# Kernel tuning notes

Measured on AMD Instinct MI355X. Metric: run time of the kernel, lower is better.

## Reference

```python
import jax, jax.numpy as jnp
import numpy as np
from jax import lax

CONV3_NUM = 5
CONV1_NUM = 1
NEG_SLOPE = 0.2


def _leaky(x):
    return jnp.where(x >= 0, x, NEG_SLOPE * x)


def _per_sample_conv(x, k, b, pad):
    # x: [B,3,H,W], k: [B,3,3,kh,kw] (OIHW per sample), b: [B,3]
    def one(xi, ki, bi):
        y = lax.conv_general_dilated(
            xi[None], ki, (1, 1), ((pad, pad), (pad, pad)),
            dimension_numbers=("NCHW", "OIHW", "NCHW"))[0]
        return y + bi[:, None, None]
    return jax.vmap(one)(x, k, b)


def _conv3x3_block(x, feat):
    B = x.shape[0]
    k = feat[:, :81].reshape(B, 3, 3, 3, 3)
    b = feat[:, 81:84]
    return _leaky(x + _per_sample_conv(x, k, b, 1))


def _conv1x1_block(x, feat):
    B = x.shape[0]
    k = feat[:, :9].reshape(B, 3, 3, 1, 1)
    b = feat[:, 9:12]
    return _leaky(x + _per_sample_conv(x, k, b, 0))


def _att_map(f, h, w, xi):
    # f: [B,20]; h,w: [1,1,H,W]; xi: [B,1,H,W]  -> cubic trivariate polynomial
    c = lambda i: f[:, i][:, None, None, None]
    h2 = h * h; h3 = h2 * h
    w2 = w * w; w3 = w2 * w
    x2 = xi * xi; x3 = x2 * xi
    return (c(0) * h3 + c(1) * h2 * w + c(2) * h2 * xi + c(3) * h2
            + c(4) * h * w2 + c(5) * h * w * xi + c(6) * h * w
            + c(7) * h * x2 + c(8) * h * xi + c(9) * h
            + c(10) * w3 + c(11) * w2 * xi + c(12) * w2
            + c(13) * w * x2 + c(14) * w * xi + c(15) * w
            + c(16) * x3 + c(17) * x2 + c(18) * xi + c(19))


def setup_inputs() -> dict:
    key = jax.random.key(0)
    k1, k2, k3 = jax.random.split(key, 3)
    x = jax.random.normal(k1, (8, 3, 1024, 1024), dtype=jnp.float32)
    thumb_x = jax.random.normal(k2, (8, 3, 256, 256), dtype=jnp.float32)
    # meta() is an external CNN predicting per-sample params; we materialize its
    # output directly (scaled small for numerical stability of the conv stack).
    feature = jax.random.normal(k3, (8, 492), dtype=jnp.float32) * 0.05
    return {"x": x, "thumb_x": thumb_x, "feature": feature}


def reference(x, thumb_x, feature):
    B, _, H, W = x.shape
    residual = x
    for i in range(CONV3_NUM):
        x = _conv3x3_block(x, feature[:, i * 84:(i + 1) * 84])
    off = CONV3_NUM * 84
    for i in range(CONV1_NUM):
        x = _conv1x1_block(x, feature[:, off + i * 12:off + (i + 1) * 12])
    off = off + CONV1_NUM * 12
    x = residual + x
    dt = x.dtype
    h_mat = jnp.broadcast_to((jnp.arange(H, dtype=dt) / H)[None, None, :, None], (1, 1, H, W))
    w_mat = jnp.broadcast_to((jnp.arange(W, dtype=dt) / W)[None, None, None, :], (1, 1, H, W))
    atts = [_att_map(feature[:, off + 20 * c:off + 20 * (c + 1)], h_mat, w_mat, x[:, c:c + 1])
            for c in range(3)]
    att = jnp.concatenate(atts, axis=1)
    x = x * (1 + att)
    # location is None => thumbnail branch is skipped, thumb_x returned as-is
    return (x, thumb_x)
```

## Files before the change

### kernel.cpp

```cpp
#include <hip/hip_runtime.h>
#include <hip/hip_fp16.h>

typedef unsigned int uint;
typedef _Float16 h2 __attribute__((ext_vector_type(2)));


#define ROWS   42
#define W_U    23
#define CHP_U  (ROWS*W_U)
#define BUF_U  (3*CHP_U)

__device__ __forceinline__ h2   U2H(uint u) { return __builtin_bit_cast(h2, u); }
__device__ __forceinline__ uint H2U(h2 h)   { return __builtin_bit_cast(uint, h); }

__global__ void prep_weights(const float* __restrict__ feat, uint* __restrict__ wtab)
{
    const int b = blockIdx.x;
    const int t = threadIdx.x;
    float w = 0.f;
    bool valid = false;
    if (t < 405) {
        int l = t / 81, r = t % 81;
        int ic = r / 27; r %= 27;
        int ky = r / 9;  r %= 9;
        int oc = r / 3;
        int kx = r % 3;
        w = feat[b * 492 + l * 84 + ((oc * 3 + ic) * 3 + ky) * 3 + kx];
        valid = true;
    } else if (t < 420) {
        int i = t - 405;
        w = feat[b * 492 + (i / 3) * 84 + 81 + (i % 3)];
        valid = true;
    }
    if (valid) {
        _Float16 h = (_Float16)w;
        h2 hh = { h, h };
        wtab[b * 448 + t] = H2U(hh);
    }
}

__global__ __launch_bounds__(512, 8) void fused_net(
    const float* __restrict__ xin,
    const float* __restrict__ thumb,
    const float* __restrict__ feat,
    const uint*  __restrict__ wtab,
    float* __restrict__ out)
{
    const int tid = threadIdx.x;

    if (blockIdx.x == 32) {
        const int part = blockIdx.y + 32 * blockIdx.z;
        const float4* s4 = (const float4*)thumb;
        float4* d4 = (float4*)(out + 25165824ull);
        const int n4 = 1572864 / 4;
        for (int i = part * 512 + tid; i < n4; i += 256 * 512)
            d4[i] = s4[i];
        return;
    }

    const int gx0 = blockIdx.x * 32;
    const int gy0 = blockIdx.y * 32;
    const int b   = blockIdx.z;
    const float* wf = feat + b * 492;
    const uint*  wt = wtab + b * 448;

    __shared__ uint lds[2 * BUF_U + 8];
    uint* b0 = lds;
    uint* b1 = lds + BUF_U + 4;

    const float* xb = xin + ((size_t)(b * 3) << 20);
    for (int idx = tid; idx < BUF_U; idx += 512) {
        int ch  = idx / CHP_U;
        int rem = idx - ch * CHP_U;
        int row = rem / W_U;
        int u   = rem - row * W_U;
        int gy = gy0 - 5 + row;
        int gx = gx0 - 6 + 2 * u;
        float f0 = 0.f, f1 = 0.f;
        if ((unsigned)gy < 1024u) {
            const float* rp = xb + (ch << 20) + (gy << 10);
            if ((unsigned)gx < 1024u)       f0 = rp[gx];
            if ((unsigned)(gx + 1) < 1024u) f1 = rp[gx + 1];
        }
        b0[idx] = __builtin_bit_cast(uint, __builtin_amdgcn_cvt_pkrtz(f0, f1));
    }
    __syncthreads();

    const int erow = tid >> 4;
    const int col2 = (tid & 15) << 1;
    const int ub   = (5 + erow) * W_U + 3 + (col2 >> 1);
    uint resu[3];
    #pragma unroll
    for (int ch = 0; ch < 3; ++ch) resu[ch] = b0[ch * CHP_U + ub];

    const h2 c02 = { (_Float16)0.2f, (_Float16)0.2f };
    const h2 z2  = { (_Float16)0.f,  (_Float16)0.f  };

    #pragma unroll
    for (int l = 0; l < 5; ++l) {
        uint* sb = (l & 1) ? b1 : b0;
        uint* db = (l & 1) ? b0 : b1;
        const int S   = 40 - 2 * l;
        const int xs  = (S + 3) >> 2;
        const int nst = S * xs;
        const int oy  = l + 1;
        const int EX  = (l + 2) & ~1;
        if (tid < nst) {
            const int r  = tid / xs;
            const int c  = tid - r * xs;
            const int y  = oy + r;
            const int x0 = EX + 4 * c;
            const int bu = (x0 >> 1) - 1;
            const int gy  = gy0 - 5 + y;
            const int gxA = gx0 - 6 + x0;
            const uint mrow = ((unsigned)gy < 1024u) ? 0xffffffffu : 0u;
            const uint mA = mrow & ((((unsigned)gxA       < 1024u) ? 0x0000ffffu : 0u) |
                                    (((unsigned)(gxA + 1) < 1024u) ? 0xffff0000u : 0u));
            const uint mB = mrow & ((((unsigned)(gxA + 2) < 1024u) ? 0x0000ffffu : 0u) |
                                    (((unsigned)(gxA + 3) < 1024u) ? 0xffff0000u : 0u));

            h2 accA[3], accB[3];
            #pragma unroll
            for (int oc = 0; oc < 3; ++oc) {
                h2 bi = U2H(wt[405 + l * 3 + oc]);
                accA[oc] = bi; accB[oc] = bi;
            }
            uint cA[3], cB[3];
            #pragma unroll
            for (int ic = 0; ic < 3; ++ic) {
                const int ai = ic * CHP_U + (y - 1) * W_U + bu;
                #pragma unroll
                for (int ky = 0; ky < 3; ++ky) {
                    const int a = ai + ky * W_U;
                    uint u0 = sb[a], u1 = sb[a + 1], u2 = sb[a + 2], u3 = sb[a + 3];
                    uint X01 = (u0 >> 16) | (u1 << 16);
                    uint X12 = (u1 >> 16) | (u2 << 16);
                    uint X23 = (u2 >> 16) | (u3 << 16);
                    if (ky == 1) { cA[ic] = u1; cB[ic] = u2; }
                    const int wb = l * 81 + (ic * 3 + ky) * 9;
                    #pragma unroll
                    for (int oc = 0; oc < 3; ++oc) {
                        h2 w0 = U2H(wt[wb + oc * 3 + 0]);
                        h2 w1 = U2H(wt[wb + oc * 3 + 1]);
                        h2 w2 = U2H(wt[wb + oc * 3 + 2]);
                        accA[oc] = __builtin_elementwise_fma(w0, U2H(X01), accA[oc]);
                        accA[oc] = __builtin_elementwise_fma(w1, U2H(u1),  accA[oc]);
                        accA[oc] = __builtin_elementwise_fma(w2, U2H(X12), accA[oc]);
                        accB[oc] = __builtin_elementwise_fma(w0, U2H(X12), accB[oc]);
                        accB[oc] = __builtin_elementwise_fma(w1, U2H(u2),  accB[oc]);
                        accB[oc] = __builtin_elementwise_fma(w2, U2H(X23), accB[oc]);
                    }
                }
            }
            const int ob = y * W_U + (x0 >> 1);
            #pragma unroll
            for (int oc = 0; oc < 3; ++oc) {
                h2 vA = accA[oc] + U2H(cA[oc]);
                h2 vB = accB[oc] + U2H(cB[oc]);
                vA = __builtin_elementwise_fma(c02, __builtin_elementwise_min(vA, z2),
                                               __builtin_elementwise_max(vA, z2));
                vB = __builtin_elementwise_fma(c02, __builtin_elementwise_min(vB, z2),
                                               __builtin_elementwise_max(vB, z2));
                db[oc * CHP_U + ob]     = H2U(vA) & mA;
                db[oc * CHP_U + ob + 1] = H2U(vB) & mB;
            }
        }
        __syncthreads();
    }

    float x5f[3][2], resf[3][2];
    #pragma unroll
    for (int ch = 0; ch < 3; ++ch) {
        h2 hr = U2H(resu[ch]);
        resf[ch][0] = (float)hr.x; resf[ch][1] = (float)hr.y;
        h2 hx = U2H(b1[ch * CHP_U + ub]);
        x5f[ch][0] = (float)hx.x; x5f[ch][1] = (float)hx.y;
    }
    const int gy = gy0 + erow;
    const float h1 = (float)gy * (1.0f / 1024.0f);
    const float h2v = h1 * h1, h3 = h2v * h1;
    float* outb = out + ((size_t)(b * 3) << 20);
    float tmp[3][2];
    #pragma unroll
    for (int j = 0; j < 2; ++j) {
        const float wc = (float)(gx0 + col2 + j) * (1.0f / 1024.0f);
        const float w2 = wc * wc, w3 = w2 * wc;
        const float hw = h1 * wc, h2w = h2v * wc, hw2 = h1 * w2;
        #pragma unroll
        for (int oc = 0; oc < 3; ++oc) {
            float s = x5f[oc][j] + wf[429 + oc]
                    + wf[420 + oc * 3 + 0] * x5f[0][j]
                    + wf[420 + oc * 3 + 1] * x5f[1][j]
                    + wf[420 + oc * 3 + 2] * x5f[2][j];
            s = s >= 0.f ? s : 0.2f * s;
            const float xf = resf[oc][j] + s;
            const float x1 = xf, x2 = x1 * x1, x3 = x2 * x1;
            const float* cf = wf + 432 + oc * 20;
            float att =
                cf[0] * h3 + cf[1] * h2w + cf[2] * h2v * x1 + cf[3] * h2v +
                cf[4] * hw2 + cf[5] * hw * x1 + cf[6] * hw + cf[7] * h1 * x2 +
                cf[8] * h1 * x1 + cf[9] * h1 + cf[10] * w3 + cf[11] * w2 * x1 +
                cf[12] * w2 + cf[13] * wc * x2 + cf[14] * wc * x1 + cf[15] * wc +
                cf[16] * x3 + cf[17] * x2 + cf[18] * x1 + cf[19];
            tmp[oc][j] = xf * (1.f + att);
        }
    }
    #pragma unroll
    for (int oc = 0; oc < 3; ++oc) {
        float2 v = {tmp[oc][0], tmp[oc][1]};
        *(float2*)&outb[((size_t)oc << 20) + ((size_t)gy << 10) + (gx0 + col2)] = v;
    }
}

extern "C" void kernel_launch(void* const* d_in, const int* in_sizes, int n_in,
                              void* d_out, int out_size, void* d_ws, size_t ws_size,
                              hipStream_t stream) {
    const float* x     = (const float*)d_in[0];
    const float* thumb = (const float*)d_in[1];
    const float* feat  = (const float*)d_in[2];
    float* out = (float*)d_out;
    uint* wtab = (uint*)d_ws;

    prep_weights<<<dim3(8), 448, 0, stream>>>(feat, wtab);
    dim3 grid(33, 32, 8);
    fused_net<<<grid, 512, 0, stream>>>(x, thumb, feat, wtab, out);
}
```

Baseline: 299.2 us.

## Compute two output rows per thread in conv layers, vectorize loads, specialize edge tiles

Each thread now computes a 2-row by 4-column patch. It reads 4 input rows per channel instead of 6, which cuts LDS loads and shift ops for the overlapping vertical window. The tile load uses float2 global reads, with a fast path for interior tiles that skips bounds checks. Masking is applied only on edge tiles, and the row stride is padded from 23 to 26 to change LDS bank mapping. LeakyReLU becomes max(v, 0.2v) and the residual add is folded into the accumulators. Fewer threads are active per layer and register pressure per thread goes up.

```diff
diff --git a/kernel.cpp b/kernel.cpp
--- a/kernel.cpp
+++ b/kernel.cpp
@@ -6,7 +6,8 @@
 
 
 #define ROWS   42
-#define W_U    23
+#define W_U    26
+#define W_REAL 23
 #define CHP_U  (ROWS*W_U)
 #define BUF_U  (3*CHP_U)
 
@@ -61,6 +62,7 @@
     const int gx0 = blockIdx.x * 32;
     const int gy0 = blockIdx.y * 32;
     const int b   = blockIdx.z;
+    const bool edge = (gx0 == 0) | (gx0 == 992) | (gy0 == 0) | (gy0 == 992);
     const float* wf = feat + b * 492;
     const uint*  wt = wtab + b * 448;
 
@@ -69,20 +71,32 @@
     uint* b1 = lds + BUF_U + 4;
 
     const float* xb = xin + ((size_t)(b * 3) << 20);
-    for (int idx = tid; idx < BUF_U; idx += 512) {
-        int ch  = idx / CHP_U;
-        int rem = idx - ch * CHP_U;
-        int row = rem / W_U;
-        int u   = rem - row * W_U;
-        int gy = gy0 - 5 + row;
-        int gx = gx0 - 6 + 2 * u;
-        float f0 = 0.f, f1 = 0.f;
-        if ((unsigned)gy < 1024u) {
-            const float* rp = xb + (ch << 20) + (gy << 10);
-            if ((unsigned)gx < 1024u)       f0 = rp[gx];
-            if ((unsigned)(gx + 1) < 1024u) f1 = rp[gx + 1];
-        }
-        b0[idx] = __builtin_bit_cast(uint, __builtin_amdgcn_cvt_pkrtz(f0, f1));
+    if (!edge) {
+        for (int idx = tid; idx < 3 * ROWS * W_REAL; idx += 512) {
+            int ch  = idx / (ROWS * W_REAL);
+            int rem = idx - ch * (ROWS * W_REAL);
+            int row = rem / W_REAL;
+            int u   = rem - row * W_REAL;
+            const float2 f = *(const float2*)(xb + ((size_t)ch << 20) +
+                                              ((size_t)(gy0 - 5 + row) << 10) +
+                                              (gx0 - 6 + 2 * u));
+            b0[ch * CHP_U + row * W_U + u] =
+                __builtin_bit_cast(uint, __builtin_amdgcn_cvt_pkrtz(f.x, f.y));
+        }
+    } else {
+        for (int idx = tid; idx < 3 * ROWS * W_REAL; idx += 512) {
+            int ch  = idx / (ROWS * W_REAL);
+            int rem = idx - ch * (ROWS * W_REAL);
+            int row = rem / W_REAL;
+            int u   = rem - row * W_REAL;
+            const int gy = gy0 - 5 + row;
+            const int gx = gx0 - 6 + 2 * u;
+            float2 f = {0.f, 0.f};
+            if ((unsigned)gy < 1024u && (unsigned)gx < 1024u)
+                f = *(const float2*)(xb + ((size_t)ch << 20) + ((size_t)gy << 10) + gx);
+            b0[ch * CHP_U + row * W_U + u] =
+                __builtin_bit_cast(uint, __builtin_amdgcn_cvt_pkrtz(f.x, f.y));
+        }
     }
     __syncthreads();
 
@@ -94,75 +108,97 @@
     for (int ch = 0; ch < 3; ++ch) resu[ch] = b0[ch * CHP_U + ub];
 
     const h2 c02 = { (_Float16)0.2f, (_Float16)0.2f };
-    const h2 z2  = { (_Float16)0.f,  (_Float16)0.f  };
 
     #pragma unroll
     for (int l = 0; l < 5; ++l) {
         uint* sb = (l & 1) ? b1 : b0;
         uint* db = (l & 1) ? b0 : b1;
         const int S   = 40 - 2 * l;
+        const int R   = S >> 1;
         const int xs  = (S + 3) >> 2;
-        const int nst = S * xs;
+        const int nst = R * xs;
         const int oy  = l + 1;
         const int EX  = (l + 2) & ~1;
         if (tid < nst) {
             const int r  = tid / xs;
             const int c  = tid - r * xs;
-            const int y  = oy + r;
+            const int y0 = oy + 2 * r;
             const int x0 = EX + 4 * c;
             const int bu = (x0 >> 1) - 1;
-            const int gy  = gy0 - 5 + y;
-            const int gxA = gx0 - 6 + x0;
-            const uint mrow = ((unsigned)gy < 1024u) ? 0xffffffffu : 0u;
-            const uint mA = mrow & ((((unsigned)gxA       < 1024u) ? 0x0000ffffu : 0u) |
-                                    (((unsigned)(gxA + 1) < 1024u) ? 0xffff0000u : 0u));
-            const uint mB = mrow & ((((unsigned)(gxA + 2) < 1024u) ? 0x0000ffffu : 0u) |
-                                    (((unsigned)(gxA + 3) < 1024u) ? 0xffff0000u : 0u));
-
-            h2 accA[3], accB[3];
+
+            h2 accA[2][3], accB[2][3];
             #pragma unroll
             for (int oc = 0; oc < 3; ++oc) {
-                h2 bi = U2H(wt[405 + l * 3 + oc]);
-                accA[oc] = bi; accB[oc] = bi;
+                const h2 bi = U2H(wt[405 + l * 3 + oc]);
+                accA[0][oc] = bi; accA[1][oc] = bi;
+                accB[0][oc] = bi; accB[1][oc] = bi;
             }
-            uint cA[3], cB[3];
             #pragma unroll
             for (int ic = 0; ic < 3; ++ic) {
-                const int ai = ic * CHP_U + (y - 1) * W_U + bu;
+                const int ai = ic * CHP_U + (y0 - 1) * W_U + bu;
                 #pragma unroll
-                for (int ky = 0; ky < 3; ++ky) {
-                    const int a = ai + ky * W_U;
-                    uint u0 = sb[a], u1 = sb[a + 1], u2 = sb[a + 2], u3 = sb[a + 3];
-                    uint X01 = (u0 >> 16) | (u1 << 16);
-                    uint X12 = (u1 >> 16) | (u2 << 16);
-                    uint X23 = (u2 >> 16) | (u3 << 16);
-                    if (ky == 1) { cA[ic] = u1; cB[ic] = u2; }
-                    const int wb = l * 81 + (ic * 3 + ky) * 9;
+                for (int t = 0; t < 4; ++t) {
+                    const int a = ai + t * W_U;
+                    const uint u0 = sb[a], u1 = sb[a + 1], u2 = sb[a + 2], u3 = sb[a + 3];
+                    const h2 X01 = U2H((u0 >> 16) | (u1 << 16));
+                    const h2 C1  = U2H(u1);
+                    const h2 X12 = U2H((u1 >> 16) | (u2 << 16));
+                    const h2 C2  = U2H(u2);
+                    const h2 X23 = U2H((u2 >> 16) | (u3 << 16));
+                    #pragma unroll
+                    for (int j = 0; j < 2; ++j) {
+                        const int ky = t - j;
+                        if (0 <= ky && ky <= 2) {
+                            const int wb = l * 81 + (ic * 3 + ky) * 9;
+                            #pragma unroll
+                            for (int oc = 0; oc < 3; ++oc) {
+                                const h2 w0 = U2H(wt[wb + oc * 3 + 0]);
+                                const h2 w1 = U2H(wt[wb + oc * 3 + 1]);
+                                const h2 w2 = U2H(wt[wb + oc * 3 + 2]);
+                                accA[j][oc] = __builtin_elementwise_fma(w0, X01, accA[j][oc]);
+                                accA[j][oc] = __builtin_elementwise_fma(w1, C1,  accA[j][oc]);
+                                accA[j][oc] = __builtin_elementwise_fma(w2, X12, accA[j][oc]);
+                                accB[j][oc] = __builtin_elementwise_fma(w0, X12, accB[j][oc]);
+                                accB[j][oc] = __builtin_elementwise_fma(w1, C2,  accB[j][oc]);
+                                accB[j][oc] = __builtin_elementwise_fma(w2, X23, accB[j][oc]);
+                            }
+                        }
+                    }
+                    if (t == 1) { accA[0][ic] += C1; accB[0][ic] += C2; }
+                    if (t == 2) { accA[1][ic] += C1; accB[1][ic] += C2; }
+                }
+            }
+            const int obase = y0 * W_U + (x0 >> 1);
+            if (!edge) {
+                #pragma unroll
+                for (int j = 0; j < 2; ++j) {
                     #pragma unroll
                     for (int oc = 0; oc < 3; ++oc) {
-                        h2 w0 = U2H(wt[wb + oc * 3 + 0]);
-                        h2 w1 = U2H(wt[wb + oc * 3 + 1]);
-                        h2 w2 = U2H(wt[wb + oc * 3 + 2]);
-                        accA[oc] = __builtin_elementwise_fma(w0, U2H(X01), accA[oc]);
-                        accA[oc] = __builtin_elementwise_fma(w1, U2H(u1),  accA[oc]);
-                        accA[oc] = __builtin_elementwise_fma(w2, U2H(X12), accA[oc]);
-                        accB[oc] = __builtin_elementwise_fma(w0, U2H(X12), accB[oc]);
-                        accB[oc] = __builtin_elementwise_fma(w1, U2H(u2),  accB[oc]);
-                        accB[oc] = __builtin_elementwise_fma(w2, U2H(X23), accB[oc]);
+                        h2 vA = accA[j][oc]; vA = __builtin_elementwise_max(vA, c02 * vA);
+                        h2 vB = accB[j][oc]; vB = __builtin_elementwise_max(vB, c02 * vB);
+                        db[oc * CHP_U + obase + j * W_U]     = H2U(vA);
+                        db[oc * CHP_U + obase + j * W_U + 1] = H2U(vB);
                     }
                 }
-            }
-            const int ob = y * W_U + (x0 >> 1);
-            #pragma unroll
-            for (int oc = 0; oc < 3; ++oc) {
-                h2 vA = accA[oc] + U2H(cA[oc]);
-                h2 vB = accB[oc] + U2H(cB[oc]);
-                vA = __builtin_elementwise_fma(c02, __builtin_elementwise_min(vA, z2),
-                                               __builtin_elementwise_max(vA, z2));
-                vB = __builtin_elementwise_fma(c02, __builtin_elementwise_min(vB, z2),
-                                               __builtin_elementwise_max(vB, z2));
-                db[oc * CHP_U + ob]     = H2U(vA) & mA;
-                db[oc * CHP_U + ob + 1] = H2U(vB) & mB;
+            } else {
+                const int gy  = gy0 - 5 + y0;
+                const int gxA = gx0 - 6 + x0;
+                const uint mA0 = ((((unsigned)gxA       < 1024u) ? 0x0000ffffu : 0u) |
+                                  (((unsigned)(gxA + 1) < 1024u) ? 0xffff0000u : 0u));
+                const uint mB0 = ((((unsigned)(gxA + 2) < 1024u) ? 0x0000ffffu : 0u) |
+                                  (((unsigned)(gxA + 3) < 1024u) ? 0xffff0000u : 0u));
+                #pragma unroll
+                for (int j = 0; j < 2; ++j) {
+                    const uint mrow = ((unsigned)(gy + j) < 1024u) ? 0xffffffffu : 0u;
+                    const uint mA = mrow & mA0, mB = mrow & mB0;
+                    #pragma unroll
+                    for (int oc = 0; oc < 3; ++oc) {
+                        h2 vA = accA[j][oc]; vA = __builtin_elementwise_max(vA, c02 * vA);
+                        h2 vB = accB[j][oc]; vB = __builtin_elementwise_max(vB, c02 * vB);
+                        db[oc * CHP_U + obase + j * W_U]     = H2U(vA) & mA;
+                        db[oc * CHP_U + obase + j * W_U + 1] = H2U(vB) & mB;
+                    }
+                }
             }
         }
         __syncthreads();
```

Measured after the change: 301.4 us. About the same (+0.7%).
